# Kernel optimization log

Hardware: AMD Instinct MI355X
Metric: run time of the kernel (lower is better)

The kernel has to match this reference:

```python
import jax, jax.numpy as jnp
import numpy as np

B, C, T = 8, 1024, 4096
H, K = 16, 15          # n_heads, kernel_size
PAD = K // 2           # 'same' padding so output length == T


def setup_inputs() -> dict:
    key = jax.random.key(0)
    k1, k2 = jax.random.split(key)
    x = jax.random.normal(k1, (B, C, T), dtype=jnp.float32)
    # weight_linear: Linear(C -> H*K, bias=False); scaled small for sane softmax
    W_lin = jax.random.normal(k2, (H * K, C), dtype=jnp.float32) * 0.02
    return {"x": x, "W_lin": W_lin}


def reference(x, W_lin):
    """Dynamic lightweight conv: per-(b,t) softmax kernels applied depthwise.
    x: (B, C, T) -> (B, C, T). Channel c uses head c % H (matches view(-1,H,T)).
    """
    Bb, Cc, Tt = x.shape
    R = Cc // H
    # kernel generation: (B,T,H,K), softmax over taps K
    proj = jnp.einsum('bct,fc->btf', x, W_lin).reshape(Bb, Tt, H, K)
    w = jax.nn.softmax(proj, axis=-1)
    w = jnp.transpose(w, (0, 2, 3, 1))            # (B, H, K, T)
    # group channels by head: c = r*H + h  ->  head h = c % H
    xr = x.reshape(Bb, R, H, Tt)                  # (B, R, H, T)
    xpad = jnp.pad(xr, ((0, 0), (0, 0), (0, 0), (PAD, PAD)))
    out = jnp.zeros_like(xr)
    for k in range(K):  # small fixed tap count; avoids (B,C,T,K) unfold blowup
        out = out + w[:, None, :, k, :] * xpad[..., k:k + Tt]
    return out.reshape(Bb, Cc, Tt)
```

## Files before the change

### kernel.cpp

```cpp
#include <hip/hip_runtime.h>
#include <hip/hip_bf16.h>

constexpr int Bn  = 8;
constexpr int Cn  = 1024;
constexpr int Tn  = 4096;
constexpr int Hn  = 16;
constexpr int Kn  = 15;
constexpr int Fp  = 256;

typedef __attribute__((ext_vector_type(8))) short    bf16x8;
typedef __attribute__((ext_vector_type(4))) float    f32x4;

static __device__ __forceinline__ unsigned short f2bf(float f) {
    __hip_bfloat16 h = __float2bfloat16(f);
    return *reinterpret_cast<unsigned short*>(&h);
}

__global__ __launch_bounds__(256)
void lwc_wpad(const float* __restrict__ W, unsigned short* __restrict__ Wp)
{
    const int idx = (blockIdx.x * 256 + threadIdx.x) * 4;
    const int m = idx >> 10, c = idx & 1023;
    const int h = m >> 4, k = m & 15;
    float4 v = make_float4(0.f, 0.f, 0.f, 0.f);
    if (k < 15)
        v = *reinterpret_cast<const float4*>(W + ((size_t)(h * 15 + k)) * Cn + c);
    ushort4 o;
    o.x = f2bf(v.x); o.y = f2bf(v.y); o.z = f2bf(v.z); o.w = f2bf(v.w);
    *reinterpret_cast<ushort4*>(Wp + idx) = o;
}

__global__ __launch_bounds__(256)
void lwc_fused_weights(const float* __restrict__ x,
                       const unsigned short* __restrict__ Wp,
                       float* __restrict__ wout)
{
    __shared__ __align__(16) unsigned short xs[2 * 16 * 64 * 8];

    const int tid  = threadIdx.x;
    const int lane = tid & 63;
    const int wv   = tid >> 6;
    const int t0   = blockIdx.x * 64;
    const int b    = blockIdx.y;

    const int lr = lane & 15;
    const int lg = lane >> 4;

    const int tcell = tid & 15;
    const int coct  = tid >> 4;
    const float* xbase = x + (size_t)b * Cn * Tn + t0 + tcell * 4;

    f32x4 acc[4][4];
#pragma unroll
    for (int i = 0; i < 4; ++i)
#pragma unroll
        for (int j = 0; j < 4; ++j) acc[i][j] = (f32x4){0.f, 0.f, 0.f, 0.f};

    float4 ld[8];
#pragma unroll
    for (int j = 0; j < 8; ++j)
        ld[j] = *reinterpret_cast<const float4*>(
            xbase + (size_t)(coct * 8 + j) * Tn);

    const unsigned short* Abase = Wp + ((size_t)(wv * 64 + lr)) * Cn + lg * 8;
    const int lrx0 = lr ^ lg;
    unsigned short* wrow = xs + coct * 512;
    const int csw = coct & 7;

#pragma unroll 1
    for (int ck = 0; ck < 8; ++ck) {
        const int buf = (ck & 1) * 8192;

        float cf[8][4];
#pragma unroll
        for (int j = 0; j < 8; ++j) {
            cf[j][0] = ld[j].x; cf[j][1] = ld[j].y;
            cf[j][2] = ld[j].z; cf[j][3] = ld[j].w;
        }
#pragma unroll
        for (int tt = 0; tt < 4; ++tt) {
            const int slot  = tcell * 4 + tt;
            const int slotw = slot ^ csw;
            bf16x8 pk;
#pragma unroll
            for (int j = 0; j < 8; ++j) pk[j] = (short)f2bf(cf[j][tt]);
            *reinterpret_cast<bf16x8*>(wrow + buf + slotw * 8) = pk;
        }

        __syncthreads();

        if (ck < 7) {
#pragma unroll
            for (int j = 0; j < 8; ++j)
                ld[j] = *reinterpret_cast<const float4*>(
                    xbase + (size_t)((ck + 1) * 128 + coct * 8 + j) * Tn);
        }

        const unsigned short* Apc = Abase + ck * 128;
#pragma unroll
        for (int ks = 0; ks < 4; ++ks) {
            bf16x8 af[4], bfr[4];
            const unsigned short* ap = Apc + ks * 32;
#pragma unroll
            for (int mi = 0; mi < 4; ++mi)
                af[mi] = *reinterpret_cast<const bf16x8*>(ap + (size_t)mi * 16 * Cn);
            const int lrx = lrx0 ^ ((ks & 1) << 2);
            const unsigned short* bp = xs + buf + (ks * 4 + lg) * 512 + lrx * 8;
#pragma unroll
            for (int ni = 0; ni < 4; ++ni)
                bfr[ni] = *reinterpret_cast<const bf16x8*>(bp + ni * 128);
#pragma unroll
            for (int mi = 0; mi < 4; ++mi)
#pragma unroll
                for (int ni = 0; ni < 4; ++ni)
                    acc[mi][ni] = __builtin_amdgcn_mfma_f32_16x16x32_bf16(
                        af[mi], bfr[ni], acc[mi][ni], 0, 0, 0);
        }
    }

    const int tcol = lane & 15;
#pragma unroll
    for (int mi = 0; mi < 4; ++mi) {
        const int h = wv * 4 + mi;
        float* hbase = wout + (((size_t)b * Hn + h) * Kn) * Tn + t0;
#pragma unroll
        for (int ni = 0; ni < 4; ++ni) {
            f32x4 v = acc[mi][ni];
            float mx = -3.0e38f;
#pragma unroll
            for (int r = 0; r < 4; ++r)
                if (lg * 4 + r < 15) mx = fmaxf(mx, v[r]);
            mx = fmaxf(mx, __shfl_xor(mx, 16));
            mx = fmaxf(mx, __shfl_xor(mx, 32));
            float e[4], s = 0.f;
#pragma unroll
            for (int r = 0; r < 4; ++r) {
                const int k = lg * 4 + r;
                e[r] = (k < 15) ? __expf(v[r] - mx) : 0.f;
                s += e[r];
            }
            s += __shfl_xor(s, 16);
            s += __shfl_xor(s, 32);
            const float inv = 1.f / s;
#pragma unroll
            for (int r = 0; r < 4; ++r) {
                const int k = lg * 4 + r;
                if (k < 15)
                    hbase[(size_t)k * Tn + ni * 16 + tcol] = e[r] * inv;
            }
        }
    }
}

__global__ __launch_bounds__(256)
void lwc_apply(const float* __restrict__ x,
               const float* __restrict__ w,
               float* __restrict__ out)
{
    const int tid = threadIdx.x;
    const int t0  = blockIdx.x * 1024;
    const int h   = blockIdx.y >> 2;
    const int rq  = blockIdx.y & 3;
    const int b   = blockIdx.z;
    const int tb  = 4 * tid;

    float4 wreg[15];
#pragma unroll
    for (int k = 0; k < 15; ++k)
        wreg[k] = *reinterpret_cast<const float4*>(
            w + (((size_t)b * Hn + h) * Kn + k) * Tn + t0 + tb);

    const int g0 = t0 + tb - 8;
    const bool interior = (g0 >= 0) && (g0 + 20 <= Tn);

#pragma unroll 2
    for (int rr = 0; rr < 16; ++rr) {
        const int c = (rq * 16 + rr) * Hn + h;
        const float* xrow = x + ((size_t)b * Cn + c) * Tn;

        float xv[20];
        if (interior) {
            const float4* xp = reinterpret_cast<const float4*>(xrow + g0);
#pragma unroll
            for (int q = 0; q < 5; ++q) {
                const float4 a = xp[q];
                xv[4 * q + 0] = a.x; xv[4 * q + 1] = a.y;
                xv[4 * q + 2] = a.z; xv[4 * q + 3] = a.w;
            }
        } else {
#pragma unroll
            for (int i = 0; i < 20; ++i) {
                const int g = g0 + i;
                xv[i] = ((unsigned)g < (unsigned)Tn) ? xrow[g] : 0.f;
            }
        }

        float ox = 0.f, oy = 0.f, oz = 0.f, ow = 0.f;
#pragma unroll
        for (int k = 0; k < 15; ++k) {
            ox += wreg[k].x * xv[k + 1];
            oy += wreg[k].y * xv[k + 2];
            oz += wreg[k].z * xv[k + 3];
            ow += wreg[k].w * xv[k + 4];
        }
        float4 o; o.x = ox; o.y = oy; o.z = oz; o.w = ow;
        *reinterpret_cast<float4*>(out + ((size_t)b * Cn + c) * Tn + t0 + tb) = o;
    }
}

extern "C" void kernel_launch(void* const* d_in, const int* in_sizes, int n_in,
                              void* d_out, int out_size, void* d_ws, size_t ws_size,
                              hipStream_t stream)
{
    const float* x = (const float*)d_in[0];
    const float* W = (const float*)d_in[1];
    float* out     = (float*)d_out;
    float* wks     = (float*)d_ws;

    unsigned short* Wp = (unsigned short*)d_out;

    lwc_wpad<<<dim3(Fp * Cn / 4 / 256), 256, 0, stream>>>(W, Wp);

    dim3 gF(Tn / 64, Bn);
    lwc_fused_weights<<<gF, 256, 0, stream>>>(x, Wp, wks);

    dim3 gB(Tn / 1024, Hn * 4, Bn);
    lwc_apply<<<gB, 256, 0, stream>>>(x, wks, out);
}
```

Before: 120.2 us.

## Fuse softmax kernel generation and depthwise apply into one kernel via LDS

Merges the projection+softmax kernel with the apply kernel so the per-(b,t) softmax weights are kept in shared memory instead of round-tripping through a global workspace. Each block now covers 64 timesteps for all 1024 channels, reading x a second time for the apply phase (likely L2-resident). The double-buffered LDS staging is replaced by a single buffer with an extra barrier, and launch bounds request 2 blocks per CU. Risks: less parallelism per block in the apply phase (512 blocks, each doing 64 channel rows sequentially), lost overlap in the GEMM loop, and higher LDS use.

```diff
diff --git a/kernel.cpp b/kernel.cpp
--- a/kernel.cpp
+++ b/kernel.cpp
@@ -30,12 +30,13 @@
     *reinterpret_cast<ushort4*>(Wp + idx) = o;
 }
 
-__global__ __launch_bounds__(256)
-void lwc_fused_weights(const float* __restrict__ x,
-                       const unsigned short* __restrict__ Wp,
-                       float* __restrict__ wout)
+__global__ __launch_bounds__(256, 2)
+void lwc_full(const float* __restrict__ x,
+              const unsigned short* __restrict__ Wp,
+              float* __restrict__ out)
 {
-    __shared__ __align__(16) unsigned short xs[2 * 16 * 64 * 8];
+    __shared__ __align__(16) unsigned short xs[16 * 64 * 8];
+    __shared__ __align__(16) float wl[Hn * Kn * 64];
 
     const int tid  = threadIdx.x;
     const int lane = tid & 63;
@@ -63,36 +64,32 @@
             xbase + (size_t)(coct * 8 + j) * Tn);
 
     const unsigned short* Abase = Wp + ((size_t)(wv * 64 + lr)) * Cn + lg * 8;
+    unsigned short* wrow = xs + coct * 512;
+    const int csw  = coct & 7;
     const int lrx0 = lr ^ lg;
-    unsigned short* wrow = xs + coct * 512;
-    const int csw = coct & 7;
 
 #pragma unroll 1
     for (int ck = 0; ck < 8; ++ck) {
-        const int buf = (ck & 1) * 8192;
-
-        float cf[8][4];
-#pragma unroll
-        for (int j = 0; j < 8; ++j) {
-            cf[j][0] = ld[j].x; cf[j][1] = ld[j].y;
-            cf[j][2] = ld[j].z; cf[j][3] = ld[j].w;
-        }
 #pragma unroll
         for (int tt = 0; tt < 4; ++tt) {
-            const int slot  = tcell * 4 + tt;
-            const int slotw = slot ^ csw;
+            const int slotw = (tcell * 4 + tt) ^ csw;
+            float cf[8] = {0};
+#pragma unroll
+            for (int j = 0; j < 8; ++j)
+                cf[j] = (tt == 0) ? ld[j].x : (tt == 1) ? ld[j].y
+                      : (tt == 2) ? ld[j].z : ld[j].w;
             bf16x8 pk;
 #pragma unroll
-            for (int j = 0; j < 8; ++j) pk[j] = (short)f2bf(cf[j][tt]);
-            *reinterpret_cast<bf16x8*>(wrow + buf + slotw * 8) = pk;
-        }
-
+            for (int j = 0; j < 8; ++j) pk[j] = (short)f2bf(cf[j]);
+            *reinterpret_cast<bf16x8*>(wrow + slotw * 8) = pk;
+        }
         __syncthreads();
 
+        float4 ldn[8];
         if (ck < 7) {
 #pragma unroll
             for (int j = 0; j < 8; ++j)
-                ld[j] = *reinterpret_cast<const float4*>(
+                ldn[j] = *reinterpret_cast<const float4*>(
                     xbase + (size_t)((ck + 1) * 128 + coct * 8 + j) * Tn);
         }
 
@@ -105,7 +102,7 @@
             for (int mi = 0; mi < 4; ++mi)
                 af[mi] = *reinterpret_cast<const bf16x8*>(ap + (size_t)mi * 16 * Cn);
             const int lrx = lrx0 ^ ((ks & 1) << 2);
-            const unsigned short* bp = xs + buf + (ks * 4 + lg) * 512 + lrx * 8;
+            const unsigned short* bp = xs + (ks * 4 + lg) * 512 + lrx * 8;
 #pragma unroll
             for (int ni = 0; ni < 4; ++ni)
                 bfr[ni] = *reinterpret_cast<const bf16x8*>(bp + ni * 128);
@@ -116,13 +113,19 @@
                     acc[mi][ni] = __builtin_amdgcn_mfma_f32_16x16x32_bf16(
                         af[mi], bfr[ni], acc[mi][ni], 0, 0, 0);
         }
+        __syncthreads();
+
+        if (ck < 7) {
+#pragma unroll
+            for (int j = 0; j < 8; ++j) ld[j] = ldn[j];
+        }
     }
 
     const int tcol = lane & 15;
 #pragma unroll
     for (int mi = 0; mi < 4; ++mi) {
         const int h = wv * 4 + mi;
-        float* hbase = wout + (((size_t)b * Hn + h) * Kn) * Tn + t0;
+        float* hb = wl + h * 960;
 #pragma unroll
         for (int ni = 0; ni < 4; ++ni) {
             f32x4 v = acc[mi][ni];
@@ -146,37 +149,29 @@
             for (int r = 0; r < 4; ++r) {
                 const int k = lg * 4 + r;
                 if (k < 15)
-                    hbase[(size_t)k * Tn + ni * 16 + tcol] = e[r] * inv;
+                    hb[k * 64 + ni * 16 + tcol] = e[r] * inv;
             }
         }
     }
-}
-
-__global__ __launch_bounds__(256)
-void lwc_apply(const float* __restrict__ x,
-               const float* __restrict__ w,
-               float* __restrict__ out)
-{
-    const int tid = threadIdx.x;
-    const int t0  = blockIdx.x * 1024;
-    const int h   = blockIdx.y >> 2;
-    const int rq  = blockIdx.y & 3;
-    const int b   = blockIdx.z;
-    const int tb  = 4 * tid;
+    __syncthreads();
+
+    const int h2 = tid >> 4;
+    const int tq = tid & 15;
 
     float4 wreg[15];
 #pragma unroll
     for (int k = 0; k < 15; ++k)
-        wreg[k] = *reinterpret_cast<const float4*>(
-            w + (((size_t)b * Hn + h) * Kn + k) * Tn + t0 + tb);
-
-    const int g0 = t0 + tb - 8;
+        wreg[k] = *reinterpret_cast<const float4*>(wl + h2 * 960 + k * 64 + tq * 4);
+
+    const int g0 = t0 + tq * 4 - 8;
     const bool interior = (g0 >= 0) && (g0 + 20 <= Tn);
+    const float* xb2 = x + (size_t)b * Cn * Tn;
+    float*       ob2 = out + (size_t)b * Cn * Tn + t0 + tq * 4;
 
 #pragma unroll 2
-    for (int rr = 0; rr < 16; ++rr) {
-        const int c = (rq * 16 + rr) * Hn + h;
-        const float* xrow = x + ((size_t)b * Cn + c) * Tn;
+    for (int rr = 0; rr < 64; ++rr) {
+        const int c = rr * 16 + h2;
+        const float* xrow = xb2 + (size_t)c * Tn;
 
         float xv[20];
         if (interior) {
@@ -204,7 +199,7 @@
             ow += wreg[k].w * xv[k + 4];
         }
         float4 o; o.x = ox; o.y = oy; o.z = oz; o.w = ow;
-        *reinterpret_cast<float4*>(out + ((size_t)b * Cn + c) * Tn + t0 + tb) = o;
+        *reinterpret_cast<float4*>(ob2 + (size_t)c * Tn) = o;
     }
 }
 
@@ -215,15 +210,11 @@
     const float* x = (const float*)d_in[0];
     const float* W = (const float*)d_in[1];
     float* out     = (float*)d_out;
-    float* wks     = (float*)d_ws;
-
-    unsigned short* Wp = (unsigned short*)d_out;
+
+    unsigned short* Wp = (unsigned short*)d_ws;
 
     lwc_wpad<<<dim3(Fp * Cn / 4 / 256), 256, 0, stream>>>(W, Wp);
 
     dim3 gF(Tn / 64, Bn);
-    lwc_fused_weights<<<gF, 256, 0, stream>>>(x, Wp, wks);
-
-    dim3 gB(Tn / 1024, Hn * 4, Bn);
-    lwc_apply<<<gB, 256, 0, stream>>>(x, wks, out);
-}
+    lwc_full<<<gF, 256, 0, stream>>>(x, Wp, out);
+}
```

Result: slower. 140.4 us (+16.8%).
